# Kernel tuning notes

Hardware: AMD Instinct MI355X
Metric: run time of the kernel (lower is better)

Reference implementation:

```python
import jax, jax.numpy as jnp
import numpy as np
from jax import lax

B, S, E = 8, 2048, 1024
NH, K = 4, 4
DH = E // NH  # 256


def setup_inputs() -> dict:
    key = jax.random.key(0)
    ks = jax.random.split(key, 8)
    sc = 0.02  # small_init-style scale
    return {
        "x": jax.random.normal(ks[0], (B, S, E), jnp.float32),
        "conv_w": jax.random.normal(ks[1], (K, 1, E), jnp.float32) * sc,  # depthwise (W,1,E)
        "conv_b": jnp.zeros((E,), jnp.float32),
        "fgate_w": jax.random.normal(ks[2], (NH, DH, DH), jnp.float32) * sc,
        "igate_w": jax.random.normal(ks[3], (NH, DH, DH), jnp.float32) * sc,
        "zgate_w": jax.random.normal(ks[4], (NH, DH, DH), jnp.float32) * sc,
        "ogate_w": jax.random.normal(ks[5], (NH, DH, DH), jnp.float32) * sc,
        "rkernel": jax.random.normal(ks[6], (NH, DH, 4 * DH), jnp.float32) * sc,
        "rbias": jnp.zeros((NH, 4, DH), jnp.float32),
        "gn_weight": jnp.ones((E,), jnp.float32),
    }


def _headwise(x, w):
    # LinearHeadwiseExpand, bias=False: einsum('...hd,hod->...ho')
    Bx, Sx, _ = x.shape
    return jnp.einsum('bshd,hod->bsho', x.reshape(Bx, Sx, NH, DH), w)


def reference(x, conv_w, conv_b, fgate_w, igate_w, zgate_w, ogate_w, rkernel, rbias, gn_weight):
    # --- causal depthwise conv1d + SiLU ---
    xp = jnp.pad(x, ((0, 0), (K - 1, 0), (0, 0)))  # left pad -> causal
    xc = lax.conv_general_dilated(
        xp, conv_w, window_strides=(1,), padding='VALID',
        dimension_numbers=('NWC', 'WIO', 'NWC'), feature_group_count=E) + conv_b
    x_conv = xc * jax.nn.sigmoid(xc)  # SiLU

    # --- headwise gate pre-activations (matches torch cat order [i,f,z,o]) ---
    gi = _headwise(x_conv, fgate_w)
    gf = _headwise(x_conv, igate_w)
    gz = _headwise(x, zgate_w)
    go = _headwise(x, ogate_w)
    gx = jnp.stack([gi, gf, gz, go], axis=3)      # (B,S,NH,4,DH)
    gx_t = jnp.moveaxis(gx, 1, 0)                 # (S,B,NH,4,DH)

    # --- stabilized exponential-gated sLSTM recurrence (xLSTM vanilla cell) ---
    z0 = jnp.zeros((B, NH, DH), x.dtype)

    def step(carry, xt):
        y, c, n, m = carry  # each (B,NH,DH)
        ry = jnp.einsum('bhd,hdk->bhk', y, rkernel).reshape(B, NH, 4, DH)
        raw = xt + ry + rbias
        ir, fr, zr, orr = raw[:, :, 0], raw[:, :, 1], raw[:, :, 2], raw[:, :, 3]
        logfplusm = m + jax.nn.log_sigmoid(fr)
        mnew = jnp.maximum(ir, logfplusm)
        ig = jnp.exp(ir - mnew)
        fg = jnp.exp(logfplusm - mnew)
        cnew = fg * c + ig * jnp.tanh(zr)
        nnew = fg * n + ig
        ynew = jax.nn.sigmoid(orr) * cnew / nnew
        return (ynew, cnew, nnew, mnew), ynew

    _, ys = lax.scan(step, (z0, z0, z0, z0), gx_t)  # ys: (S,B,NH,DH)
    y = jnp.moveaxis(ys, 0, 1)                       # (B,S,NH,DH)

    # --- MultiHeadLayerNorm: group_norm with num_groups=NH, weight only (no bias) ---
    mu = jnp.mean(y, axis=-1, keepdims=True)
    var = jnp.var(y, axis=-1, keepdims=True)
    yn = (y - mu) * lax.rsqrt(var + 1e-5)
    out = (yn * gn_weight.reshape(NH, DH)).reshape(B, S, E)
    return out
```

## Files before the change

kernel.cpp:

```cpp
#include <hip/hip_runtime.h>
#include <hip/hip_fp16.h>

#define BB 8
#define SS 2048
#define EE 1024
#define NHH 4
#define DHH 256

__device__ __forceinline__ __half2 u2h2(unsigned int u) {
  union { unsigned int u; __half2 h; } c; c.u = u; return c.h;
}
__device__ __forceinline__ unsigned int h2u(__half2 h) {
  union { unsigned int u; __half2 h; } c; c.h = h; return c.u;
}

__global__ __launch_bounds__(256) void gates_gemm(
    const float* __restrict__ x, const float* __restrict__ conv_w,
    const float* __restrict__ conv_b,
    const float* __restrict__ fgw, const float* __restrict__ igw,
    const float* __restrict__ zgw, const float* __restrict__ ogw,
    __half* __restrict__ gx)
{
  __shared__ float Xs[67][33];
  __shared__ float As[64][33];
  __shared__ float Bs[32][68];

  const int tid = threadIdx.x;
  const int mt = blockIdx.x;
  const int nt = blockIdx.y;
  const int p  = blockIdx.z;
  const int h  = p >> 1, pair = p & 1;
  const int b  = mt >> 5;
  const int s0 = (mt & 31) << 6;
  const int n0 = nt << 6;

  const float* W0 = pair ? zgw : fgw;
  const float* W1 = pair ? ogw : igw;

  const int tx = tid & 15, ty = tid >> 4;
  float acc[4][4] = {};

  for (int d0 = 0; d0 < DHH; d0 += 32) {
    for (int i = tid; i < 67 * 32; i += 256) {
      int r = i >> 5, c = i & 31;
      int s = s0 - 3 + r;
      float v = 0.f;
      if (s >= 0) v = x[((size_t)b * SS + s) * EE + h * DHH + d0 + c];
      Xs[r][c] = v;
    }
    for (int i = tid; i < 32 * 64; i += 256) {
      int j = i >> 5, c = i & 31;
      int o = n0 + j;
      const float* Wp = (o < 256) ? W0 : W1;
      int oo = o & 255;
      Bs[c][j] = Wp[((size_t)h * DHH + oo) * DHH + d0 + c];
    }
    __syncthreads();
    if (pair == 0) {
      for (int i = tid; i < 64 * 32; i += 256) {
        int r = i >> 5, c = i & 31;
        int e = h * DHH + d0 + c;
        float xc = conv_b[e];
        xc = fmaf(Xs[r + 0][c], conv_w[0 * EE + e], xc);
        xc = fmaf(Xs[r + 1][c], conv_w[1 * EE + e], xc);
        xc = fmaf(Xs[r + 2][c], conv_w[2 * EE + e], xc);
        xc = fmaf(Xs[r + 3][c], conv_w[3 * EE + e], xc);
        float sg = 1.f / (1.f + __expf(-xc));
        As[r][c] = xc * sg;
      }
    } else {
      for (int i = tid; i < 64 * 32; i += 256) {
        int r = i >> 5, c = i & 31;
        As[r][c] = Xs[r + 3][c];
      }
    }
    __syncthreads();
#pragma unroll
    for (int kk = 0; kk < 32; ++kk) {
      float a[4];
#pragma unroll
      for (int i = 0; i < 4; ++i) a[i] = As[ty * 4 + i][kk];
      float4 bv = *(const float4*)&Bs[kk][tx * 4];
      float bb[4] = {bv.x, bv.y, bv.z, bv.w};
#pragma unroll
      for (int i = 0; i < 4; ++i)
#pragma unroll
        for (int j = 0; j < 4; ++j)
          acc[i][j] = fmaf(a[i], bb[j], acc[i][j]);
    }
    __syncthreads();
  }

#pragma unroll
  for (int i = 0; i < 4; ++i) {
    int s = s0 + ty * 4 + i;
    size_t base = (((size_t)s * BB + b) * NHH + h) * 1024 + (size_t)pair * 512 + n0 + tx * 4;
    uint2 st;
    st.x = h2u(__floats2half2_rn(acc[i][0], acc[i][1]));
    st.y = h2u(__floats2half2_rn(acc[i][2], acc[i][3]));
    *(uint2*)(gx + base) = st;
  }
}

__global__
__attribute__((amdgpu_flat_work_group_size(512, 512), amdgpu_waves_per_eu(1)))
void slstm_scan(
    const float* __restrict__ rk,
    const float* __restrict__ rb,
    const __half* __restrict__ gx,
    float* __restrict__ out)
{
  extern __shared__ unsigned char smem[];
  uint4* wl4   = (uint4*)smem;
  __half* ypub = (__half*)(smem + 131072);

  const int t = threadIdx.x;
  const int b = blockIdx.x >> 2, h = blockIdx.x & 3;
  const int d = t >> 1, par = t & 1;
  const int k0 = par * 256 + d;
  const int k1 = 512 + par * 256 + d;
  const float* Rh = rk + (size_t)h * DHH * 1024;

  __half2 w0[128];
  __half2 w1r[64];
#pragma unroll
  for (int pp = 0; pp < 128; ++pp)
    w0[pp] = __floats2half2_rn(Rh[(2 * pp) * 1024 + k0], Rh[(2 * pp + 1) * 1024 + k0]);
#pragma unroll
  for (int pp = 0; pp < 64; ++pp)
    w1r[pp] = __floats2half2_rn(Rh[(2 * pp) * 1024 + k1], Rh[(2 * pp + 1) * 1024 + k1]);
  for (int q = 0; q < 16; ++q) {
    uint4 u;
    u.x = h2u(__floats2half2_rn(Rh[(128 + 8 * q + 0) * 1024 + k1],
                                Rh[(128 + 8 * q + 1) * 1024 + k1]));
    u.y = h2u(__floats2half2_rn(Rh[(128 + 8 * q + 2) * 1024 + k1],
                                Rh[(128 + 8 * q + 3) * 1024 + k1]));
    u.z = h2u(__floats2half2_rn(Rh[(128 + 8 * q + 4) * 1024 + k1],
                                Rh[(128 + 8 * q + 5) * 1024 + k1]));
    u.w = h2u(__floats2half2_rn(Rh[(128 + 8 * q + 6) * 1024 + k1],
                                Rh[(128 + 8 * q + 7) * 1024 + k1]));
    wl4[q * 512 + t] = u;
  }
  const float rb0 = rb[h * 1024 + k0];
  const float rb1 = rb[h * 1024 + k1];
  float c = 0.f, n = 0.f, m = 0.f;
  if (t < 256) { ypub[t] = __float2half(0.f); ypub[256 + t] = __float2half(0.f); }
  __syncthreads();

  int cur = 0;
  const __half* pg = gx + ((size_t)b * NHH + h) * 1024;
  float cx0 = __half2float(pg[k0]);
  float cx1 = __half2float(pg[k1]);
  const __half2 hz = __floats2half2_rn(0.f, 0.f);
  const size_t out_base = ((size_t)b * SS) * EE + h * DHH + d;

  for (int st = 0; st < SS; ++st) {
    const __half* pn = pg + ((st + 1 < SS) ? (size_t)(BB * NHH * 1024) : 0);
    const __half nx0 = pn[k0];
    const __half nx1 = pn[k1];

    const uint4* yv = (const uint4*)(ypub + cur * 256);
    __half2 s0a = hz, s0b = hz, s1a = hz, s1b = hz;
#pragma unroll
    for (int j = 0; j < 16; ++j) {
      uint4 yq = yv[j];
      __half2 y0 = u2h2(yq.x), y1 = u2h2(yq.y), y2 = u2h2(yq.z), y3 = u2h2(yq.w);
      s0a = __hfma2(w0[4 * j + 0], y0, s0a);
      s1a = __hfma2(w1r[4 * j + 0], y0, s1a);
      s0b = __hfma2(w0[4 * j + 1], y1, s0b);
      s1b = __hfma2(w1r[4 * j + 1], y1, s1b);
      s0a = __hfma2(w0[4 * j + 2], y2, s0a);
      s1a = __hfma2(w1r[4 * j + 2], y2, s1a);
      s0b = __hfma2(w0[4 * j + 3], y3, s0b);
      s1b = __hfma2(w1r[4 * j + 3], y3, s1b);
    }
#pragma unroll
    for (int j = 16; j < 32; ++j) {
      uint4 yq = yv[j];
      uint4 wq = wl4[(j - 16) * 512 + t];
      __half2 y0 = u2h2(yq.x), y1 = u2h2(yq.y), y2 = u2h2(yq.z), y3 = u2h2(yq.w);
      s0a = __hfma2(w0[4 * j + 0], y0, s0a);
      s1a = __hfma2(u2h2(wq.x), y0, s1a);
      s0b = __hfma2(w0[4 * j + 1], y1, s0b);
      s1b = __hfma2(u2h2(wq.y), y1, s1b);
      s0a = __hfma2(w0[4 * j + 2], y2, s0a);
      s1a = __hfma2(u2h2(wq.z), y2, s1a);
      s0b = __hfma2(w0[4 * j + 3], y3, s0b);
      s1b = __hfma2(u2h2(wq.w), y3, s1b);
    }

    float acc0 = __low2float(s0a) + __high2float(s0a) + __low2float(s0b) + __high2float(s0b);
    float acc1 = __low2float(s1a) + __high2float(s1a) + __low2float(s1b) + __high2float(s1b);
    float raw0 = acc0 + cx0 + rb0;
    float raw1 = acc1 + cx1 + rb1;

    float pr0 = __shfl_xor(raw0, 1);
    float pr1 = __shfl_xor(raw1, 1);
    float iv = par ? pr0 : raw0;
    float fv = par ? raw0 : pr0;
    float zv = par ? pr1 : raw1;
    float ov = par ? raw1 : pr1;

    float ea = __expf(-fabsf(fv));
    float ls = fminf(fv, 0.f) - __logf(1.f + ea);
    float lfm = m + ls;
    float mn = fmaxf(iv, lfm);
    float ig = __expf(iv - mn);
    float fg = __expf(lfm - mn);
    float pz = __expf(-2.f * fabsf(zv));
    float tmag = __fdividef(1.f - pz, 1.f + pz);
    float th = (zv < 0.f) ? -tmag : tmag;
    c = fg * c + ig * th;
    n = fg * n + ig;
    float og = __fdividef(1.f, 1.f + __expf(-ov));
    float y = og * __fdividef(c, n);
    m = mn;

    if (par == 0) {
      out[out_base + (size_t)st * EE] = y;
      ypub[(cur ^ 1) * 256 + d] = __float2half(y);
    }
    __syncthreads();
    cur ^= 1;
    pg = pn;
    cx0 = __half2float(nx0);
    cx1 = __half2float(nx1);
  }
}

__global__ __launch_bounds__(256) void groupnorm(
    float* __restrict__ y, const float* __restrict__ gnw)
{
  const int row = blockIdx.x;
  const int t = threadIdx.x;
  float4 v = ((const float4*)y)[(size_t)row * 256 + t];
  float s = v.x + v.y + v.z + v.w;
  float q = v.x * v.x + v.y * v.y + v.z * v.z + v.w * v.w;
#pragma unroll
  for (int mask = 1; mask < 64; mask <<= 1) {
    s += __shfl_xor(s, mask, 64);
    q += __shfl_xor(q, mask, 64);
  }
  float mu = s * (1.f / 256.f);
  float var = q * (1.f / 256.f) - mu * mu;
  float rs = rsqrtf(var + 1e-5f);
  float4 g = ((const float4*)gnw)[t];
  float4 o;
  o.x = (v.x - mu) * rs * g.x;
  o.y = (v.y - mu) * rs * g.y;
  o.z = (v.z - mu) * rs * g.z;
  o.w = (v.w - mu) * rs * g.w;
  ((float4*)y)[(size_t)row * 256 + t] = o;
}

extern "C" void kernel_launch(void* const* d_in, const int* in_sizes, int n_in,
                              void* d_out, int out_size, void* d_ws, size_t ws_size,
                              hipStream_t stream) {
  const float* x      = (const float*)d_in[0];
  const float* conv_w = (const float*)d_in[1];
  const float* conv_b = (const float*)d_in[2];
  const float* fgw    = (const float*)d_in[3];
  const float* igw    = (const float*)d_in[4];
  const float* zgw    = (const float*)d_in[5];
  const float* ogw    = (const float*)d_in[6];
  const float* rk     = (const float*)d_in[7];
  const float* rb     = (const float*)d_in[8];
  const float* gnw    = (const float*)d_in[9];
  float* out = (float*)d_out;
  __half* gx = (__half*)d_ws;

  dim3 g1(256, 8, 8);
  gates_gemm<<<g1, 256, 0, stream>>>(x, conv_w, conv_b, fgw, igw, zgw, ogw, gx);

  const int scan_lds = 131072 + 1024;
  (void)hipFuncSetAttribute(reinterpret_cast<const void*>(slstm_scan),
                            hipFuncAttributeMaxDynamicSharedMemorySize, scan_lds);
  slstm_scan<<<32, 512, scan_lds, stream>>>(rk, rb, gx, out);

  groupnorm<<<BB * SS, 256, 0, stream>>>(out, gnw);
}
```

Before: 4.416 ms.

## Split recurrent matvec along K across thread pairs using fp32-accumulating fdot2

Reorganizes the per-step recurrent matvec so each thread pair splits the reduction (K) dimension instead of the output gate columns. Each thread now computes partial sums for all four gates over half of the hidden vector and combines them with one shuffle per gate. Products are accumulated with the packed fp16 dot-product instruction into fp32, instead of packed half FMAs with fp16 accumulators. This halves the y loads per thread and improves accumulation precision. In exchange, both lanes of a pair redundantly run the gate nonlinearities and there are four shuffles instead of two.

```diff
diff --git a/kernel.cpp b/kernel.cpp
--- a/kernel.cpp
+++ b/kernel.cpp
@@ -7,11 +7,28 @@
 #define NHH 4
 #define DHH 256
 
+typedef _Float16 f16x2 __attribute__((ext_vector_type(2)));
+
 __device__ __forceinline__ __half2 u2h2(unsigned int u) {
   union { unsigned int u; __half2 h; } c; c.u = u; return c.h;
 }
 __device__ __forceinline__ unsigned int h2u(__half2 h) {
   union { unsigned int u; __half2 h; } c; c.h = h; return c.u;
+}
+__device__ __forceinline__ f16x2 u2f(unsigned int u) {
+  union { unsigned int u; f16x2 f; } c; c.u = u; return c.f;
+}
+__device__ __forceinline__ unsigned int pack2(float a, float b) {
+  f16x2 f; f.x = (_Float16)a; f.y = (_Float16)b;
+  union { f16x2 f; unsigned int u; } c; c.f = f; return c.u;
+}
+__device__ __forceinline__ float fdot2u(unsigned int w, unsigned int y, float acc) {
+#if __has_builtin(__builtin_amdgcn_fdot2)
+  return __builtin_amdgcn_fdot2(u2f(w), u2f(y), acc, false);
+#else
+  __half2 a = u2h2(w), b = u2h2(y);
+  return acc + __low2float(a) * __low2float(b) + __high2float(a) * __high2float(b);
+#endif
 }
 
 __global__ __launch_bounds__(256) void gates_gemm(
@@ -117,90 +134,86 @@
   const int t = threadIdx.x;
   const int b = blockIdx.x >> 2, h = blockIdx.x & 3;
   const int d = t >> 1, par = t & 1;
-  const int k0 = par * 256 + d;
-  const int k1 = 512 + par * 256 + d;
+  const int kbase = par << 7;
   const float* Rh = rk + (size_t)h * DHH * 1024;
 
-  __half2 w0[128];
-  __half2 w1r[64];
-#pragma unroll
-  for (int pp = 0; pp < 128; ++pp)
-    w0[pp] = __floats2half2_rn(Rh[(2 * pp) * 1024 + k0], Rh[(2 * pp + 1) * 1024 + k0]);
-#pragma unroll
-  for (int pp = 0; pp < 64; ++pp)
-    w1r[pp] = __floats2half2_rn(Rh[(2 * pp) * 1024 + k1], Rh[(2 * pp + 1) * 1024 + k1]);
-  for (int q = 0; q < 16; ++q) {
-    uint4 u;
-    u.x = h2u(__floats2half2_rn(Rh[(128 + 8 * q + 0) * 1024 + k1],
-                                Rh[(128 + 8 * q + 1) * 1024 + k1]));
-    u.y = h2u(__floats2half2_rn(Rh[(128 + 8 * q + 2) * 1024 + k1],
-                                Rh[(128 + 8 * q + 3) * 1024 + k1]));
-    u.z = h2u(__floats2half2_rn(Rh[(128 + 8 * q + 4) * 1024 + k1],
-                                Rh[(128 + 8 * q + 5) * 1024 + k1]));
-    u.w = h2u(__floats2half2_rn(Rh[(128 + 8 * q + 6) * 1024 + k1],
-                                Rh[(128 + 8 * q + 7) * 1024 + k1]));
-    wl4[q * 512 + t] = u;
-  }
-  const float rb0 = rb[h * 1024 + k0];
-  const float rb1 = rb[h * 1024 + k1];
+  unsigned int wv[3][64];
+#pragma unroll
+  for (int g = 0; g < 3; ++g) {
+    const int col = g * 256 + d;
+#pragma unroll
+    for (int pp = 0; pp < 64; ++pp) {
+      int k = kbase + 2 * pp;
+      wv[g][pp] = pack2(Rh[(size_t)k * 1024 + col], Rh[(size_t)(k + 1) * 1024 + col]);
+    }
+  }
+  {
+    const int col = 3 * 256 + d;
+    for (int q = 0; q < 16; ++q) {
+      uint4 u;
+      int k = kbase + 8 * q;
+      u.x = pack2(Rh[(size_t)(k + 0) * 1024 + col], Rh[(size_t)(k + 1) * 1024 + col]);
+      u.y = pack2(Rh[(size_t)(k + 2) * 1024 + col], Rh[(size_t)(k + 3) * 1024 + col]);
+      u.z = pack2(Rh[(size_t)(k + 4) * 1024 + col], Rh[(size_t)(k + 5) * 1024 + col]);
+      u.w = pack2(Rh[(size_t)(k + 6) * 1024 + col], Rh[(size_t)(k + 7) * 1024 + col]);
+      wl4[q * 512 + t] = u;
+    }
+  }
+
+  float rbv[4];
+#pragma unroll
+  for (int g = 0; g < 4; ++g) rbv[g] = rb[h * 1024 + g * 256 + d];
+
   float c = 0.f, n = 0.f, m = 0.f;
   if (t < 256) { ypub[t] = __float2half(0.f); ypub[256 + t] = __float2half(0.f); }
   __syncthreads();
 
   int cur = 0;
   const __half* pg = gx + ((size_t)b * NHH + h) * 1024;
-  float cx0 = __half2float(pg[k0]);
-  float cx1 = __half2float(pg[k1]);
-  const __half2 hz = __floats2half2_rn(0.f, 0.f);
+  float cx[4];
+#pragma unroll
+  for (int g = 0; g < 4; ++g) cx[g] = __half2float(pg[g * 256 + d]);
   const size_t out_base = ((size_t)b * SS) * EE + h * DHH + d;
 
   for (int st = 0; st < SS; ++st) {
     const __half* pn = pg + ((st + 1 < SS) ? (size_t)(BB * NHH * 1024) : 0);
-    const __half nx0 = pn[k0];
-    const __half nx1 = pn[k1];
-
-    const uint4* yv = (const uint4*)(ypub + cur * 256);
-    __half2 s0a = hz, s0b = hz, s1a = hz, s1b = hz;
+    __half nx[4];
+#pragma unroll
+    for (int g = 0; g < 4; ++g) nx[g] = pn[g * 256 + d];
+
+    const uint4* yv = (const uint4*)(ypub + cur * 256) + (par << 4);
+    float aA0 = 0.f, aB0 = 0.f, aA1 = 0.f, aB1 = 0.f;
+    float aA2 = 0.f, aB2 = 0.f, aA3 = 0.f, aB3 = 0.f;
 #pragma unroll
     for (int j = 0; j < 16; ++j) {
       uint4 yq = yv[j];
-      __half2 y0 = u2h2(yq.x), y1 = u2h2(yq.y), y2 = u2h2(yq.z), y3 = u2h2(yq.w);
-      s0a = __hfma2(w0[4 * j + 0], y0, s0a);
-      s1a = __hfma2(w1r[4 * j + 0], y0, s1a);
-      s0b = __hfma2(w0[4 * j + 1], y1, s0b);
-      s1b = __hfma2(w1r[4 * j + 1], y1, s1b);
-      s0a = __hfma2(w0[4 * j + 2], y2, s0a);
-      s1a = __hfma2(w1r[4 * j + 2], y2, s1a);
-      s0b = __hfma2(w0[4 * j + 3], y3, s0b);
-      s1b = __hfma2(w1r[4 * j + 3], y3, s1b);
-    }
-#pragma unroll
-    for (int j = 16; j < 32; ++j) {
-      uint4 yq = yv[j];
-      uint4 wq = wl4[(j - 16) * 512 + t];
-      __half2 y0 = u2h2(yq.x), y1 = u2h2(yq.y), y2 = u2h2(yq.z), y3 = u2h2(yq.w);
-      s0a = __hfma2(w0[4 * j + 0], y0, s0a);
-      s1a = __hfma2(u2h2(wq.x), y0, s1a);
-      s0b = __hfma2(w0[4 * j + 1], y1, s0b);
-      s1b = __hfma2(u2h2(wq.y), y1, s1b);
-      s0a = __hfma2(w0[4 * j + 2], y2, s0a);
-      s1a = __hfma2(u2h2(wq.z), y2, s1a);
-      s0b = __hfma2(w0[4 * j + 3], y3, s0b);
-      s1b = __hfma2(u2h2(wq.w), y3, s1b);
-    }
-
-    float acc0 = __low2float(s0a) + __high2float(s0a) + __low2float(s0b) + __high2float(s0b);
-    float acc1 = __low2float(s1a) + __high2float(s1a) + __low2float(s1b) + __high2float(s1b);
-    float raw0 = acc0 + cx0 + rb0;
-    float raw1 = acc1 + cx1 + rb1;
-
-    float pr0 = __shfl_xor(raw0, 1);
-    float pr1 = __shfl_xor(raw1, 1);
-    float iv = par ? pr0 : raw0;
-    float fv = par ? raw0 : pr0;
-    float zv = par ? pr1 : raw1;
-    float ov = par ? raw1 : pr1;
-
+      uint4 wq = wl4[j * 512 + t];
+      aA0 = fdot2u(wv[0][4 * j + 0], yq.x, aA0);
+      aA1 = fdot2u(wv[1][4 * j + 0], yq.x, aA1);
+      aA2 = fdot2u(wv[2][4 * j + 0], yq.x, aA2);
+      aA3 = fdot2u(wq.x,             yq.x, aA3);
+      aB0 = fdot2u(wv[0][4 * j + 1], yq.y, aB0);
+      aB1 = fdot2u(wv[1][4 * j + 1], yq.y, aB1);
+      aB2 = fdot2u(wv[2][4 * j + 1], yq.y, aB2);
+      aB3 = fdot2u(wq.y,             yq.y, aB3);
+      aA0 = fdot2u(wv[0][4 * j + 2], yq.z, aA0);
+      aA1 = fdot2u(wv[1][4 * j + 2], yq.z, aA1);
+      aA2 = fdot2u(wv[2][4 * j + 2], yq.z, aA2);
+      aA3 = fdot2u(wq.z,             yq.z, aA3);
+      aB0 = fdot2u(wv[0][4 * j + 3], yq.w, aB0);
+      aB1 = fdot2u(wv[1][4 * j + 3], yq.w, aB1);
+      aB2 = fdot2u(wv[2][4 * j + 3], yq.w, aB2);
+      aB3 = fdot2u(wq.w,             yq.w, aB3);
+    }
+
+    float part0 = aA0 + aB0, part1 = aA1 + aB1;
+    float part2 = aA2 + aB2, part3 = aA3 + aB3;
+    float raw0 = part0 + __shfl_xor(part0, 1) + cx[0] + rbv[0];
+    float raw1 = part1 + __shfl_xor(part1, 1) + cx[1] + rbv[1];
+    float raw2 = part2 + __shfl_xor(part2, 1) + cx[2] + rbv[2];
+    float raw3 = part3 + __shfl_xor(part3, 1) + cx[3] + rbv[3];
+
+    float iv = raw0, fv = raw1, zv = raw2, ov = raw3;
     float ea = __expf(-fabsf(fv));
     float ls = fminf(fv, 0.f) - __logf(1.f + ea);
     float lfm = m + ls;
@@ -223,8 +236,8 @@
     __syncthreads();
     cur ^= 1;
     pg = pn;
-    cx0 = __half2float(nx0);
-    cx1 = __half2float(nx1);
+#pragma unroll
+    for (int g = 0; g < 4; ++g) cx[g] = __half2float(nx[g]);
   }
 }
 
```

New measurement: 4.292 ms. 1.03x faster.
